# Kernel tuning notes

Measured on AMD Instinct MI355X. Metric: run time of the kernel, lower is better.

The kernel has to match this reference:

```python
import jax, jax.numpy as jnp
import numpy as np

EPS = 1e-5


def setup_inputs() -> dict:
    key = jax.random.key(0)
    k0, k1, k2, k3 = jax.random.split(key, 4)
    B, C, H, W = 64, 128, 64, 64
    x = jax.random.normal(k0, (B, C, H, W), dtype=jnp.float32)
    w = jax.random.normal(k1, (C, C, 1), dtype=jnp.float32) * 0.05  # conv1d kernel_size=1 weight
    b = jax.random.normal(k2, (C,), dtype=jnp.float32) * 0.05       # conv1d bias
    s = jax.random.normal(k3, (1, C, 1), dtype=jnp.float32)         # learned per-channel gate logits
    offset = jnp.ones((1,), dtype=jnp.float32) * 8.0                 # module inits offset to 8
    return {"x": x, "w": w, "b": b, "s": s, "offset": offset}


def reference(x, w, b, s, offset):
    B, C, H, W = x.shape
    HW = H * W
    # Checkerboard mask: mask[c, l] = (c + l) % 2  (even channel -> [0,1,0,1,...])
    c_idx = jnp.arange(C)
    l_idx = jnp.arange(HW)
    mask = ((c_idx[:, None] + l_idx[None, :]) % 2).astype(x.dtype)  # (C, HW)

    x_flat = x.reshape(B, C, HW)
    x_masked = x_flat * mask                                         # (B, C, HW)
    # 1x1 conv1d: pointwise channel mix + bias
    z = jnp.einsum('oc,bcl->bol', w[:, :, 0], x_masked) + b[None, :, None]
    pool = z.mean(axis=1)                                            # avgpool over channels -> (B, HW)
    g = jax.nn.sigmoid(pool + offset) + EPS                          # (B, HW)
    s_sig = jax.nn.sigmoid(s[0, :, 0]) + EPS                         # (C,)

    attn_mask = (1.0 - mask)[None] * g[:, None, :] + mask[None] * s_sig[None, :, None]  # (B,C,HW)
    out = x * attn_mask.reshape(B, C, H, W)

    logdet = (C // 2) * jnp.sum(jnp.log(g), axis=-1)                 # (B,)
    logdet = logdet + B * jnp.sum(jnp.log(s_sig)[:, None] * mask)    # scalar broadcast over batch
    return out, logdet
```

## Files before the change

kernel.cpp:

```cpp
#include <hip/hip_runtime.h>
#include <hip/hip_bf16.h>
#include <math.h>


#define EPS 1e-5f
#define NC 128
#define NHW 4096
#define NB 64
#define LT 64
#define NLT (NHW / LT)


__global__ __launch_bounds__(128) void prep_kernel(const float* __restrict__ w,
                                                   const float* __restrict__ bias,
                                                   const float* __restrict__ s,
                                                   float* __restrict__ ws) {
    __shared__ float red[NC];
    const int c = threadIdx.x;
    float acc = 0.f;
    for (int o = 0; o < NC; ++o) acc += w[o * NC + c];
    ws[c] = acc * (1.f / NC);
    const float sv = s[c];
    const float ssig = 1.f / (1.f + expf(-sv)) + EPS;
    ws[NC + c] = ssig;

    red[c] = bias[c];
    __syncthreads();
    if (c == 0) {
        double sb = 0.0;
        for (int i = 0; i < NC; ++i) sb += (double)red[i];
        ws[256] = (float)(sb / NC);
    }
    __syncthreads();
    red[c] = logf(ssig);
    __syncthreads();
    if (c == 0) {
        double sl = 0.0;
        for (int i = 0; i < NC; ++i) sl += (double)red[i];
        ws[257] = (float)((double)NB * (double)(NHW / 2) * sl);
    }
}

__global__ __launch_bounds__(256) void main_kernel(const float* __restrict__ x,
                                                   const float* __restrict__ ws,
                                                   const float* __restrict__ offp,
                                                   float* __restrict__ out,
                                                   float* __restrict__ partials) {
    __shared__ float4 pp[4][16];

    const int tid  = threadIdx.x;
    const int j    = tid & 15;
    const int cg   = tid >> 4;
    const int wave = tid >> 6;
    const int lane = tid & 63;

    const int lt = blockIdx.x;
    const int b  = blockIdx.y;
    const int l0 = lt * LT;

    const size_t base = (size_t)b * (NC * NHW) + (size_t)(cg * 8) * NHW + l0 + j * 4;
    const float* __restrict__ xp = x + base;

    float4 v[8];
#pragma unroll
    for (int k = 0; k < 8; ++k)
        v[k] = *reinterpret_cast<const float4*>(xp + (size_t)k * NHW);

    float4 acc = make_float4(0.f, 0.f, 0.f, 0.f);
#pragma unroll
    for (int k = 0; k < 8; ++k) {
        const int c = cg * 8 + k;
        const float wb = ws[c];
        if (c & 1) { acc.x += wb * v[k].x; acc.z += wb * v[k].z; }
        else       { acc.y += wb * v[k].y; acc.w += wb * v[k].w; }
    }

#pragma unroll
    for (int off = 16; off <= 32; off <<= 1) {
        acc.x += __shfl_xor(acc.x, off);
        acc.y += __shfl_xor(acc.y, off);
        acc.z += __shfl_xor(acc.z, off);
        acc.w += __shfl_xor(acc.w, off);
    }
    if (lane < 16) pp[wave][j] = acc;
    __syncthreads();

    const float4 p0 = pp[0][j], p1 = pp[1][j], p2 = pp[2][j], p3 = pp[3][j];
    const float cst = ws[256] + offp[0];
    float4 g;
    g.x = 1.f / (1.f + __expf(-(p0.x + p1.x + p2.x + p3.x + cst))) + EPS;
    g.y = 1.f / (1.f + __expf(-(p0.y + p1.y + p2.y + p3.y + cst))) + EPS;
    g.z = 1.f / (1.f + __expf(-(p0.z + p1.z + p2.z + p3.z + cst))) + EPS;
    g.w = 1.f / (1.f + __expf(-(p0.w + p1.w + p2.w + p3.w + cst))) + EPS;

    if (wave == 0) {
        float slg = (lane < 16)
                  ? (__logf(g.x) + __logf(g.y) + __logf(g.z) + __logf(g.w))
                  : 0.f;
#pragma unroll
        for (int off = 32; off > 0; off >>= 1) slg += __shfl_down(slg, off);
        if (lane == 0) partials[b * gridDim.x + lt] = slg;
    }

    const float* __restrict__ ssig = ws + NC;
    float* __restrict__ op = out + base;
#pragma unroll
    for (int k = 0; k < 8; ++k) {
        const int c = cg * 8 + k;
        const float sc = ssig[c];
        float4 o;
        if (c & 1) { o.x = v[k].x * sc;  o.y = v[k].y * g.y;
                     o.z = v[k].z * sc;  o.w = v[k].w * g.w; }
        else       { o.x = v[k].x * g.x; o.y = v[k].y * sc;
                     o.z = v[k].z * g.z; o.w = v[k].w * sc; }
        *reinterpret_cast<float4*>(op + (size_t)k * NHW) = o;
    }
}

__global__ __launch_bounds__(64) void fin_kernel(const float* __restrict__ partials,
                                                 const float* __restrict__ ws,
                                                 float* __restrict__ logdet,
                                                 int nlt) {
    const int b = blockIdx.x;
    const int t = threadIdx.x;
    float v = (t < nlt) ? partials[b * nlt + t] : 0.f;
#pragma unroll
    for (int off = 32; off > 0; off >>= 1) v += __shfl_down(v, off);
    if (t == 0) logdet[b] = 64.f * v + ws[257];
}

extern "C" void kernel_launch(void* const* d_in, const int* in_sizes, int n_in,
                              void* d_out, int out_size, void* d_ws, size_t ws_size,
                              hipStream_t stream) {
    const float* x    = (const float*)d_in[0];
    const float* w    = (const float*)d_in[1];
    const float* bias = (const float*)d_in[2];
    const float* s    = (const float*)d_in[3];
    const float* offp = (const float*)d_in[4];

    float* out = (float*)d_out;
    float* logdet = out + (size_t)NB * NC * NHW;

    float* ws = (float*)d_ws;
    float* partials = ws + 512;

    const int nlt = NHW / LT;

    prep_kernel<<<1, 128, 0, stream>>>(w, bias, s, ws);
    main_kernel<<<dim3(nlt, NB), 256, 0, stream>>>(x, ws, offp, out, partials);
    fin_kernel<<<NB, 64, 0, stream>>>(partials, ws, logdet, nlt);
}
```

Measured before the change: 55.68 us.

## Fuse prep, main and finalize kernels into one with atomic logdet accumulation

Merges the three kernels into one. Each block now recomputes the column sums of the weight matrix, the channel gate sigmoids and the bias mean itself, and accumulates logdet with atomicAdd into a buffer zeroed by a memset. Output stores become nontemporal. This removes two kernel launches and the inter-kernel dependency, but every block now re-reads the full 128x128 weight matrix from cache. The float logdet sum also becomes order-nondeterministic.

```diff
diff --git a/kernel.cpp b/kernel.cpp
--- a/kernel.cpp
+++ b/kernel.cpp
@@ -10,43 +10,18 @@
 #define LT 64
 #define NLT (NHW / LT)
 
+typedef __attribute__((ext_vector_type(4))) float f4;
 
-__global__ __launch_bounds__(128) void prep_kernel(const float* __restrict__ w,
-                                                   const float* __restrict__ bias,
-                                                   const float* __restrict__ s,
-                                                   float* __restrict__ ws) {
-    __shared__ float red[NC];
-    const int c = threadIdx.x;
-    float acc = 0.f;
-    for (int o = 0; o < NC; ++o) acc += w[o * NC + c];
-    ws[c] = acc * (1.f / NC);
-    const float sv = s[c];
-    const float ssig = 1.f / (1.f + expf(-sv)) + EPS;
-    ws[NC + c] = ssig;
-
-    red[c] = bias[c];
-    __syncthreads();
-    if (c == 0) {
-        double sb = 0.0;
-        for (int i = 0; i < NC; ++i) sb += (double)red[i];
-        ws[256] = (float)(sb / NC);
-    }
-    __syncthreads();
-    red[c] = logf(ssig);
-    __syncthreads();
-    if (c == 0) {
-        double sl = 0.0;
-        for (int i = 0; i < NC; ++i) sl += (double)red[i];
-        ws[257] = (float)((double)NB * (double)(NHW / 2) * sl);
-    }
-}
-
-__global__ __launch_bounds__(256) void main_kernel(const float* __restrict__ x,
-                                                   const float* __restrict__ ws,
-                                                   const float* __restrict__ offp,
-                                                   float* __restrict__ out,
-                                                   float* __restrict__ partials) {
+__global__ __launch_bounds__(256) void fused_kernel(const float* __restrict__ x,
+                                                    const float* __restrict__ w,
+                                                    const float* __restrict__ bias,
+                                                    const float* __restrict__ s,
+                                                    const float* __restrict__ offp,
+                                                    float* __restrict__ out,
+                                                    float* __restrict__ logdet) {
+    __shared__ float  wpart[256];
     __shared__ float4 pp[4][16];
+    __shared__ float  ls[4];
 
     const int tid  = threadIdx.x;
     const int j    = tid & 15;
@@ -66,11 +41,41 @@
     for (int k = 0; k < 8; ++k)
         v[k] = *reinterpret_cast<const float4*>(xp + (size_t)k * NHW);
 
-    float4 acc = make_float4(0.f, 0.f, 0.f, 0.f);
+    {
+        const int c  = tid & 127;
+        const int o0 = (tid >> 7) * 64;
+        const float* __restrict__ wp = w + (size_t)o0 * NC + c;
+        float a0 = 0.f, a1 = 0.f, a2 = 0.f, a3 = 0.f;
+#pragma unroll
+        for (int o = 0; o < 64; o += 4) {
+            a0 += wp[(o + 0) * NC];
+            a1 += wp[(o + 1) * NC];
+            a2 += wp[(o + 2) * NC];
+            a3 += wp[(o + 3) * NC];
+        }
+        wpart[tid] = (a0 + a1) + (a2 + a3);
+    }
+
+    float ssig[8];
+    float bias_part = 0.f;
+    float lss       = 0.f;
 #pragma unroll
     for (int k = 0; k < 8; ++k) {
-        const int c = cg * 8 + k;
-        const float wb = ws[c];
+        const int c  = cg * 8 + k;
+        const float sg = 1.f / (1.f + __expf(-s[c])) + EPS;
+        ssig[k] = sg;
+        lss += __logf(sg);
+        bias_part += bias[c];
+    }
+    bias_part *= (1.f / NC);
+
+    __syncthreads();
+
+    float4 acc = make_float4(bias_part, bias_part, bias_part, bias_part);
+#pragma unroll
+    for (int k = 0; k < 8; ++k) {
+        const int c  = cg * 8 + k;
+        const float wb = (wpart[c] + wpart[NC + c]) * (1.f / NC);
         if (c & 1) { acc.x += wb * v[k].x; acc.z += wb * v[k].z; }
         else       { acc.y += wb * v[k].y; acc.w += wb * v[k].w; }
     }
@@ -81,17 +86,19 @@
         acc.y += __shfl_xor(acc.y, off);
         acc.z += __shfl_xor(acc.z, off);
         acc.w += __shfl_xor(acc.w, off);
+        lss   += __shfl_xor(lss,   off);
     }
     if (lane < 16) pp[wave][j] = acc;
+    if (lane == 0) ls[wave] = lss;
     __syncthreads();
 
     const float4 p0 = pp[0][j], p1 = pp[1][j], p2 = pp[2][j], p3 = pp[3][j];
-    const float cst = ws[256] + offp[0];
+    const float off0 = offp[0];
     float4 g;
-    g.x = 1.f / (1.f + __expf(-(p0.x + p1.x + p2.x + p3.x + cst))) + EPS;
-    g.y = 1.f / (1.f + __expf(-(p0.y + p1.y + p2.y + p3.y + cst))) + EPS;
-    g.z = 1.f / (1.f + __expf(-(p0.z + p1.z + p2.z + p3.z + cst))) + EPS;
-    g.w = 1.f / (1.f + __expf(-(p0.w + p1.w + p2.w + p3.w + cst))) + EPS;
+    g.x = 1.f / (1.f + __expf(-(p0.x + p1.x + p2.x + p3.x + off0))) + EPS;
+    g.y = 1.f / (1.f + __expf(-(p0.y + p1.y + p2.y + p3.y + off0))) + EPS;
+    g.z = 1.f / (1.f + __expf(-(p0.z + p1.z + p2.z + p3.z + off0))) + EPS;
+    g.w = 1.f / (1.f + __expf(-(p0.w + p1.w + p2.w + p3.w + off0))) + EPS;
 
     if (wave == 0) {
         float slg = (lane < 16)
@@ -99,34 +106,24 @@
                   : 0.f;
 #pragma unroll
         for (int off = 32; off > 0; off >>= 1) slg += __shfl_down(slg, off);
-        if (lane == 0) partials[b * gridDim.x + lt] = slg;
+        if (lane == 0) {
+            const float S = ls[0] + ls[1] + ls[2] + ls[3];
+            atomicAdd(&logdet[b], 64.f * slg + 2048.f * S);
+        }
     }
 
-    const float* __restrict__ ssig = ws + NC;
     float* __restrict__ op = out + base;
 #pragma unroll
     for (int k = 0; k < 8; ++k) {
-        const int c = cg * 8 + k;
-        const float sc = ssig[c];
-        float4 o;
+        const int c  = cg * 8 + k;
+        const float sc = ssig[k];
+        f4 o;
         if (c & 1) { o.x = v[k].x * sc;  o.y = v[k].y * g.y;
                      o.z = v[k].z * sc;  o.w = v[k].w * g.w; }
         else       { o.x = v[k].x * g.x; o.y = v[k].y * sc;
                      o.z = v[k].z * g.z; o.w = v[k].w * sc; }
-        *reinterpret_cast<float4*>(op + (size_t)k * NHW) = o;
+        __builtin_nontemporal_store(o, reinterpret_cast<f4*>(op + (size_t)k * NHW));
     }
-}
-
-__global__ __launch_bounds__(64) void fin_kernel(const float* __restrict__ partials,
-                                                 const float* __restrict__ ws,
-                                                 float* __restrict__ logdet,
-                                                 int nlt) {
-    const int b = blockIdx.x;
-    const int t = threadIdx.x;
-    float v = (t < nlt) ? partials[b * nlt + t] : 0.f;
-#pragma unroll
-    for (int off = 32; off > 0; off >>= 1) v += __shfl_down(v, off);
-    if (t == 0) logdet[b] = 64.f * v + ws[257];
 }
 
 extern "C" void kernel_launch(void* const* d_in, const int* in_sizes, int n_in,
@@ -138,15 +135,10 @@
     const float* s    = (const float*)d_in[3];
     const float* offp = (const float*)d_in[4];
 
-    float* out = (float*)d_out;
+    float* out    = (float*)d_out;
     float* logdet = out + (size_t)NB * NC * NHW;
 
-    float* ws = (float*)d_ws;
-    float* partials = ws + 512;
+    hipMemsetAsync(logdet, 0, NB * sizeof(float), stream);
 
-    const int nlt = NHW / LT;
-
-    prep_kernel<<<1, 128, 0, stream>>>(w, bias, s, ws);
-    main_kernel<<<dim3(nlt, NB), 256, 0, stream>>>(x, ws, offp, out, partials);
-    fin_kernel<<<NB, 64, 0, stream>>>(partials, ws, logdet, nlt);
+    fused_kernel<<<dim3(NLT, NB), 256, 0, stream>>>(x, w, bias, s, offp, out, logdet);
 }
```

Result: slower. 61.28 us (+10.0%).
